# Kernel tuning notes

Measured on AMD Instinct MI355X. Metric: run time of the kernel, lower is better.

Reference implementation:

```python
import jax, jax.numpy as jnp
import numpy as np

EPS = 1e-8  # torch.nn.CosineSimilarity default eps
SCALE_WEIGHT = (1.0, 2.0, 3.0, 4.0)  # weight[idx] for 4 scales


def _nearest_labels(lab, H, W):
    # torch F.interpolate mode='nearest': src_idx = floor(dst_idx * in/out)
    H0, W0 = lab.shape[2], lab.shape[3]
    ri = (jnp.arange(H) * H0) // H
    ci = (jnp.arange(W) * W0) // W
    return lab[:, :, ri][:, :, :, ci]


def _scale_loss(pseudo_labels, feat, feat_old, num_class, num_old_class):
    B, C, H, W = feat.shape
    lab = _nearest_labels(pseudo_labels, H, W).reshape(-1)          # [B*H*W]
    f = jnp.transpose(feat, (0, 2, 3, 1)).reshape(-1, C)            # (b h w) c
    fo = jnp.transpose(feat_old, (0, 2, 3, 1)).reshape(-1, C)
    nf = jnp.maximum(jnp.sqrt(jnp.sum(f * f, axis=1)), EPS)
    nfo = jnp.maximum(jnp.sqrt(jnp.sum(fo * fo, axis=1)), EPS)
    sim = jnp.sum(f * fo, axis=1) / (nf * nfo)                      # per-pixel cosine
    # segment-reduce by class; label 255 (ignore) is out-of-range and dropped
    seg = jax.ops.segment_sum(sim, lab, num_segments=num_class)
    cnt = jax.ops.segment_sum(jnp.ones_like(sim), lab, num_segments=num_class)
    mean_sim = seg / jnp.maximum(cnt, 1.0)
    cls = jnp.arange(num_class)
    factor = jnp.where(cls == 0, num_old_class / num_class,
                       jnp.where(cls <= num_old_class, 1.0, 0.0))
    present = cnt > 0
    dis = 1.0 - mean_sim
    return jnp.sum(jnp.where(present, factor * dis, 0.0))


def setup_inputs() -> dict:
    key = jax.random.key(0)
    ks = jax.random.split(key, 9)
    B, C = 8, 256
    sizes = [(128, 128), (64, 64), (32, 32), (16, 16)]
    inp = {
        "pseudo_labels": jax.random.randint(ks[0], (B, 1, 512, 512), 0, 21, dtype=jnp.int64)
        if jax.config.jax_enable_x64 else
        jax.random.randint(ks[0], (B, 1, 512, 512), 0, 21).astype(jnp.int32),
    }
    for i, (h, w) in enumerate(sizes):
        inp[f"f{i}"] = jax.random.normal(ks[1 + i], (B, C, h, w), dtype=jnp.float32)
        inp[f"fo{i}"] = jax.random.normal(ks[5 + i], (B, C, h, w), dtype=jnp.float32)
    inp["num_class"] = 21
    inp["num_old_class"] = 15
    return inp


def reference(pseudo_labels, f0, f1, f2, f3, fo0, fo1, fo2, fo3, num_class, num_old_class):
    feats = (f0, f1, f2, f3)
    feats_old = (fo0, fo1, fo2, fo3)
    loss = jnp.float32(0.0)
    for idx in range(4):
        loss = loss + SCALE_WEIGHT[idx] * _scale_loss(
            pseudo_labels, feats[idx], feats_old[idx], num_class, num_old_class)
    return loss
```

## Files before the change

kernel.cpp:

```cpp
#include <hip/hip_runtime.h>
#include <math.h>


#define EPSV 1e-8f

__global__ __launch_bounds__(512)
void msrd_main(const float* __restrict__ f0, const float* __restrict__ fo0,
               const float* __restrict__ f1, const float* __restrict__ fo1,
               const float* __restrict__ f2, const float* __restrict__ fo2,
               const float* __restrict__ f3, const float* __restrict__ fo3,
               const int*   __restrict__ labels,
               const int*   __restrict__ p_nclass,
               float* __restrict__ ws)
{
    int bid = blockIdx.x;
    int scale, lb, logW, logHW, sshift;
    const float *f, *fo;
    if (bid < 1024)      { scale = 0; lb = bid;        f = f0; fo = fo0; logW = 7; logHW = 14; sshift = 2; }
    else if (bid < 1280) { scale = 1; lb = bid - 1024; f = f1; fo = fo1; logW = 6; logHW = 12; sshift = 3; }
    else if (bid < 1344) { scale = 2; lb = bid - 1280; f = f2; fo = fo2; logW = 5; logHW = 10; sshift = 4; }
    else                 { scale = 3; lb = bid - 1344; f = f3; fo = fo3; logW = 4; logHW = 8;  sshift = 5; }
    const int HW = 1 << logHW;
    const int W  = 1 << logW;

    const int tid  = threadIdx.x;
    const int wave = tid >> 6;
    const int lane = tid & 63;
    const int half = lane >> 5;
    const int gi   = lane & 31;

    const int g   = lb * 32 + gi;
    const int pix = g << 2;
    const int b   = pix >> logHW;
    const int rem = pix & (HW - 1);

    const int c0 = wave * 32 + half * 16;
    const float* __restrict__ fpb  = f  + (((size_t)(b * 256 + c0)) << logHW) + rem;
    const float* __restrict__ fopb = fo + (((size_t)(b * 256 + c0)) << logHW) + rem;

    float dx=0.f,dy=0.f,dz=0.f,dw=0.f;
    float ax=0.f,ay=0.f,az=0.f,aw=0.f;
    float bx=0.f,by=0.f,bz=0.f,bw=0.f;

    #pragma unroll
    for (int batch = 0; batch < 2; ++batch) {
        float4 X[8], Y[8];
        const size_t cb = (size_t)(batch * 8) << logHW;
        #pragma unroll
        for (int j = 0; j < 8; ++j)
            X[j] = *(const float4*)(fpb + cb + ((size_t)j << logHW));
        #pragma unroll
        for (int j = 0; j < 8; ++j)
            Y[j] = *(const float4*)(fopb + cb + ((size_t)j << logHW));
        #pragma unroll
        for (int j = 0; j < 8; ++j) {
            float4 x = X[j], y = Y[j];
            dx = fmaf(x.x, y.x, dx); dy = fmaf(x.y, y.y, dy);
            dz = fmaf(x.z, y.z, dz); dw = fmaf(x.w, y.w, dw);
            ax = fmaf(x.x, x.x, ax); ay = fmaf(x.y, x.y, ay);
            az = fmaf(x.z, x.z, az); aw = fmaf(x.w, x.w, aw);
            bx = fmaf(y.x, y.x, bx); by = fmaf(y.y, y.y, by);
            bz = fmaf(y.z, y.z, bz); bw = fmaf(y.w, y.w, bw);
        }
    }

    dx += __shfl_xor(dx, 32); dy += __shfl_xor(dy, 32);
    dz += __shfl_xor(dz, 32); dw += __shfl_xor(dw, 32);
    ax += __shfl_xor(ax, 32); ay += __shfl_xor(ay, 32);
    az += __shfl_xor(az, 32); aw += __shfl_xor(aw, 32);
    bx += __shfl_xor(bx, 32); by += __shfl_xor(by, 32);
    bz += __shfl_xor(bz, 32); bw += __shfl_xor(bw, 32);

    __shared__ float4 sD[8][32], sA[8][32], sB[8][32];
    __shared__ float bin_sim[32], bin_cnt[32];
    if (tid < 32) { bin_sim[tid] = 0.f; bin_cnt[tid] = 0.f; }
    if (half == 0) {
        sD[wave][gi] = make_float4(dx,dy,dz,dw);
        sA[wave][gi] = make_float4(ax,ay,az,aw);
        sB[wave][gi] = make_float4(bx,by,bz,bw);
    }
    __syncthreads();

    if (tid < 32) {
        float4 D = sD[0][gi], A = sA[0][gi], Bv = sB[0][gi];
        #pragma unroll
        for (int w = 1; w < 8; ++w) {
            float4 t;
            t = sD[w][gi]; D.x += t.x; D.y += t.y; D.z += t.z; D.w += t.w;
            t = sA[w][gi]; A.x += t.x; A.y += t.y; A.z += t.z; A.w += t.w;
            t = sB[w][gi]; Bv.x += t.x; Bv.y += t.y; Bv.z += t.z; Bv.w += t.w;
        }
        const int nclass  = *p_nclass;
        const int labbase = b << 18;
        float Dv[4] = {D.x, D.y, D.z, D.w};
        float Av[4] = {A.x, A.y, A.z, A.w};
        float Bw[4] = {Bv.x, Bv.y, Bv.z, Bv.w};
        #pragma unroll
        for (int j = 0; j < 4; ++j) {
            float na  = fmaxf(sqrtf(Av[j]), EPSV);
            float nb  = fmaxf(sqrtf(Bw[j]), EPSV);
            float sim = Dv[j] / (na * nb);
            int p    = rem + j;
            int h    = p >> logW;
            int col  = p & (W - 1);
            int lidx = labbase + ((h << sshift) << 9) + (col << sshift);
            int lab  = labels[lidx];
            if ((unsigned)lab < (unsigned)nclass) {
                atomicAdd(&bin_sim[lab], sim);
                atomicAdd(&bin_cnt[lab], 1.0f);
            }
        }
    }
    __syncthreads();

    if (tid < 32) {
        float s = bin_sim[tid], c = bin_cnt[tid];
        if (s != 0.f || c != 0.f) {
            atomicAdd(&ws[scale * 64 + tid],      s);
            atomicAdd(&ws[scale * 64 + 32 + tid], c);
        }
    }
}

__global__ void msrd_final(const float* __restrict__ ws,
                           const int* __restrict__ p_nclass,
                           const int* __restrict__ p_nold,
                           float* __restrict__ out)
{
    if (threadIdx.x == 0 && blockIdx.x == 0) {
        const int nc = *p_nclass;
        const int no = *p_nold;
        const float wgt[4] = {1.f, 2.f, 3.f, 4.f};
        float loss = 0.f;
        for (int s = 0; s < 4; ++s) {
            float sl = 0.f;
            for (int c = 0; c < nc && c < 32; ++c) {
                float seg = ws[s * 64 + c];
                float cnt = ws[s * 64 + 32 + c];
                if (cnt > 0.f) {
                    float factor = (c == 0) ? (float)no / (float)nc
                                            : (c <= no ? 1.f : 0.f);
                    sl += factor * (1.f - seg / fmaxf(cnt, 1.f));
                }
            }
            loss += wgt[s] * sl;
        }
        out[0] = loss;
    }
}

extern "C" void kernel_launch(void* const* d_in, const int* in_sizes, int n_in,
                              void* d_out, int out_size, void* d_ws, size_t ws_size,
                              hipStream_t stream) {
    const int*   labels = (const int*)  d_in[0];
    const float* f0  = (const float*)d_in[1];
    const float* fo0 = (const float*)d_in[2];
    const float* f1  = (const float*)d_in[3];
    const float* fo1 = (const float*)d_in[4];
    const float* f2  = (const float*)d_in[5];
    const float* fo2 = (const float*)d_in[6];
    const float* f3  = (const float*)d_in[7];
    const float* fo3 = (const float*)d_in[8];
    const int* p_nclass = (const int*)d_in[9];
    const int* p_nold   = (const int*)d_in[10];
    float* out = (float*)d_out;
    float* ws  = (float*)d_ws;

    hipMemsetAsync(ws, 0, 4 * 64 * sizeof(float), stream);
    msrd_main<<<dim3(1360), dim3(512), 0, stream>>>(f0, fo0, f1, fo1, f2, fo2, f3, fo3,
                                                    labels, p_nclass, ws);
    msrd_final<<<dim3(1), dim3(64), 0, stream>>>(ws, p_nclass, p_nold, out);
}
```

Baseline: 361.8 us.

## Halve block size, loop two channel passes per wave with smaller load batches

Each block now uses 256 threads, so every wave covers 32 channels in each of two passes instead of all channels being split across 8 waves. Loads are issued in groups of four float4 pairs with a scheduling barrier, and launch bounds request 6 waves per SIMD. The aim is lower register pressure and higher occupancy so that more memory requests are in flight. In exchange, each block has fewer loads outstanding at once and each thread carries more serial work.

```diff
diff --git a/kernel.cpp b/kernel.cpp
--- a/kernel.cpp
+++ b/kernel.cpp
@@ -4,7 +4,7 @@
 
 #define EPSV 1e-8f
 
-__global__ __launch_bounds__(512)
+__global__ __launch_bounds__(256, 6)
 void msrd_main(const float* __restrict__ f0, const float* __restrict__ fo0,
                const float* __restrict__ f1, const float* __restrict__ fo1,
                const float* __restrict__ f2, const float* __restrict__ fo2,
@@ -34,33 +34,55 @@
     const int b   = pix >> logHW;
     const int rem = pix & (HW - 1);
 
-    const int c0 = wave * 32 + half * 16;
-    const float* __restrict__ fpb  = f  + (((size_t)(b * 256 + c0)) << logHW) + rem;
-    const float* __restrict__ fopb = fo + (((size_t)(b * 256 + c0)) << logHW) + rem;
-
     float dx=0.f,dy=0.f,dz=0.f,dw=0.f;
     float ax=0.f,ay=0.f,az=0.f,aw=0.f;
     float bx=0.f,by=0.f,bz=0.f,bw=0.f;
 
     #pragma unroll
-    for (int batch = 0; batch < 2; ++batch) {
-        float4 X[8], Y[8];
-        const size_t cb = (size_t)(batch * 8) << logHW;
+    for (int pass = 0; pass < 2; ++pass) {
+        const int c0 = wave * 32 + half * 16 + pass * 128;
+        const float* __restrict__ fpb  = f  + (((size_t)(b * 256 + c0)) << logHW) + rem;
+        const float* __restrict__ fopb = fo + (((size_t)(b * 256 + c0)) << logHW) + rem;
         #pragma unroll
-        for (int j = 0; j < 8; ++j)
-            X[j] = *(const float4*)(fpb + cb + ((size_t)j << logHW));
-        #pragma unroll
-        for (int j = 0; j < 8; ++j)
-            Y[j] = *(const float4*)(fopb + cb + ((size_t)j << logHW));
-        #pragma unroll
-        for (int j = 0; j < 8; ++j) {
-            float4 x = X[j], y = Y[j];
-            dx = fmaf(x.x, y.x, dx); dy = fmaf(x.y, y.y, dy);
-            dz = fmaf(x.z, y.z, dz); dw = fmaf(x.w, y.w, dw);
-            ax = fmaf(x.x, x.x, ax); ay = fmaf(x.y, x.y, ay);
-            az = fmaf(x.z, x.z, az); aw = fmaf(x.w, x.w, aw);
-            bx = fmaf(y.x, y.x, bx); by = fmaf(y.y, y.y, by);
-            bz = fmaf(y.z, y.z, bz); bw = fmaf(y.w, y.w, bw);
+        for (int batch = 0; batch < 4; ++batch) {
+            const size_t cb = (size_t)(batch * 4) << logHW;
+            float4 X0, X1, X2, X3, Y0, Y1, Y2, Y3;
+            X0 = *(const float4*)(fpb  + cb);
+            X1 = *(const float4*)(fpb  + cb + ((size_t)1 << logHW));
+            X2 = *(const float4*)(fpb  + cb + ((size_t)2 << logHW));
+            X3 = *(const float4*)(fpb  + cb + ((size_t)3 << logHW));
+            Y0 = *(const float4*)(fopb + cb);
+            Y1 = *(const float4*)(fopb + cb + ((size_t)1 << logHW));
+            Y2 = *(const float4*)(fopb + cb + ((size_t)2 << logHW));
+            Y3 = *(const float4*)(fopb + cb + ((size_t)3 << logHW));
+            __builtin_amdgcn_sched_barrier(0);
+            dx = fmaf(X0.x, Y0.x, dx); dy = fmaf(X0.y, Y0.y, dy);
+            dz = fmaf(X0.z, Y0.z, dz); dw = fmaf(X0.w, Y0.w, dw);
+            ax = fmaf(X0.x, X0.x, ax); ay = fmaf(X0.y, X0.y, ay);
+            az = fmaf(X0.z, X0.z, az); aw = fmaf(X0.w, X0.w, aw);
+            bx = fmaf(Y0.x, Y0.x, bx); by = fmaf(Y0.y, Y0.y, by);
+            bz = fmaf(Y0.z, Y0.z, bz); bw = fmaf(Y0.w, Y0.w, bw);
+
+            dx = fmaf(X1.x, Y1.x, dx); dy = fmaf(X1.y, Y1.y, dy);
+            dz = fmaf(X1.z, Y1.z, dz); dw = fmaf(X1.w, Y1.w, dw);
+            ax = fmaf(X1.x, X1.x, ax); ay = fmaf(X1.y, X1.y, ay);
+            az = fmaf(X1.z, X1.z, az); aw = fmaf(X1.w, X1.w, aw);
+            bx = fmaf(Y1.x, Y1.x, bx); by = fmaf(Y1.y, Y1.y, by);
+            bz = fmaf(Y1.z, Y1.z, bz); bw = fmaf(Y1.w, Y1.w, bw);
+
+            dx = fmaf(X2.x, Y2.x, dx); dy = fmaf(X2.y, Y2.y, dy);
+            dz = fmaf(X2.z, Y2.z, dz); dw = fmaf(X2.w, Y2.w, dw);
+            ax = fmaf(X2.x, X2.x, ax); ay = fmaf(X2.y, X2.y, ay);
+            az = fmaf(X2.z, X2.z, az); aw = fmaf(X2.w, X2.w, aw);
+            bx = fmaf(Y2.x, Y2.x, bx); by = fmaf(Y2.y, Y2.y, by);
+            bz = fmaf(Y2.z, Y2.z, bz); bw = fmaf(Y2.w, Y2.w, bw);
+
+            dx = fmaf(X3.x, Y3.x, dx); dy = fmaf(X3.y, Y3.y, dy);
+            dz = fmaf(X3.z, Y3.z, dz); dw = fmaf(X3.w, Y3.w, dw);
+            ax = fmaf(X3.x, X3.x, ax); ay = fmaf(X3.y, X3.y, ay);
+            az = fmaf(X3.z, X3.z, az); aw = fmaf(X3.w, X3.w, aw);
+            bx = fmaf(Y3.x, Y3.x, bx); by = fmaf(Y3.y, Y3.y, by);
+            bz = fmaf(Y3.z, Y3.z, bz); bw = fmaf(Y3.w, Y3.w, bw);
         }
     }
 
@@ -71,7 +93,7 @@
     bx += __shfl_xor(bx, 32); by += __shfl_xor(by, 32);
     bz += __shfl_xor(bz, 32); bw += __shfl_xor(bw, 32);
 
-    __shared__ float4 sD[8][32], sA[8][32], sB[8][32];
+    __shared__ float4 sD[4][32], sA[4][32], sB[4][32];
     __shared__ float bin_sim[32], bin_cnt[32];
     if (tid < 32) { bin_sim[tid] = 0.f; bin_cnt[tid] = 0.f; }
     if (half == 0) {
@@ -84,7 +106,7 @@
     if (tid < 32) {
         float4 D = sD[0][gi], A = sA[0][gi], Bv = sB[0][gi];
         #pragma unroll
-        for (int w = 1; w < 8; ++w) {
+        for (int w = 1; w < 4; ++w) {
             float4 t;
             t = sD[w][gi]; D.x += t.x; D.y += t.y; D.z += t.z; D.w += t.w;
             t = sA[w][gi]; A.x += t.x; A.y += t.y; A.z += t.z; A.w += t.w;
@@ -167,7 +189,7 @@
     float* ws  = (float*)d_ws;
 
     hipMemsetAsync(ws, 0, 4 * 64 * sizeof(float), stream);
-    msrd_main<<<dim3(1360), dim3(512), 0, stream>>>(f0, fo0, f1, fo1, f2, fo2, f3, fo3,
+    msrd_main<<<dim3(1360), dim3(256), 0, stream>>>(f0, fo0, f1, fo1, f2, fo2, f3, fo3,
                                                     labels, p_nclass, ws);
     msrd_final<<<dim3(1), dim3(64), 0, stream>>>(ws, p_nclass, p_nold, out);
 }
```

Measured after the change: 387.1 us. +7.0%, slower.

## Assign one pixel per thread with full channel loop, drop cross-wave reduction

Applied to the files above, without the earlier changes.

Each block of 128 threads now handles 128 pixels, with every thread looping over all 256 channels using scalar coalesced loads. The old scheme split 16 channels per half-wave with float4 loads and combined partials through a shuffle and a shared-memory reduction. That reduction, its shared arrays and the serial 32-thread epilogue are removed, and every thread computes its cosine and does the label atomic itself. In exchange each thread runs a long dependent loop with less memory-level parallelism per block and uses narrower scalar loads. It also makes many more shared-memory atomics per block, which can contend because there are only 21 classes.

```diff
diff --git a/kernel.cpp b/kernel.cpp
--- a/kernel.cpp
+++ b/kernel.cpp
@@ -4,7 +4,7 @@
 
 #define EPSV 1e-8f
 
-__global__ __launch_bounds__(512)
+__global__ __launch_bounds__(128)
 void msrd_main(const float* __restrict__ f0, const float* __restrict__ fo0,
                const float* __restrict__ f1, const float* __restrict__ fo1,
                const float* __restrict__ f2, const float* __restrict__ fo2,
@@ -13,102 +13,59 @@
                const int*   __restrict__ p_nclass,
                float* __restrict__ ws)
 {
-    int bid = blockIdx.x;
+    const int bid = blockIdx.x;
     int scale, lb, logW, logHW, sshift;
     const float *f, *fo;
     if (bid < 1024)      { scale = 0; lb = bid;        f = f0; fo = fo0; logW = 7; logHW = 14; sshift = 2; }
     else if (bid < 1280) { scale = 1; lb = bid - 1024; f = f1; fo = fo1; logW = 6; logHW = 12; sshift = 3; }
     else if (bid < 1344) { scale = 2; lb = bid - 1280; f = f2; fo = fo2; logW = 5; logHW = 10; sshift = 4; }
     else                 { scale = 3; lb = bid - 1344; f = f3; fo = fo3; logW = 4; logHW = 8;  sshift = 5; }
-    const int HW = 1 << logHW;
-    const int W  = 1 << logW;
+    const int W   = 1 << logW;
+    const int HW  = 1 << logHW;
+    const int tid = threadIdx.x;
 
-    const int tid  = threadIdx.x;
-    const int wave = tid >> 6;
-    const int lane = tid & 63;
-    const int half = lane >> 5;
-    const int gi   = lane & 31;
-
-    const int g   = lb * 32 + gi;
-    const int pix = g << 2;
+    const int pix = lb * 128 + tid;
     const int b   = pix >> logHW;
     const int rem = pix & (HW - 1);
 
-    const int c0 = wave * 32 + half * 16;
-    const float* __restrict__ fpb  = f  + (((size_t)(b * 256 + c0)) << logHW) + rem;
-    const float* __restrict__ fopb = fo + (((size_t)(b * 256 + c0)) << logHW) + rem;
+    const float* __restrict__ fp  = f  + (((size_t)(b * 256)) << logHW) + rem;
+    const float* __restrict__ fop = fo + (((size_t)(b * 256)) << logHW) + rem;
+    const size_t cs = (size_t)HW;
 
-    float dx=0.f,dy=0.f,dz=0.f,dw=0.f;
-    float ax=0.f,ay=0.f,az=0.f,aw=0.f;
-    float bx=0.f,by=0.f,bz=0.f,bw=0.f;
+    float d = 0.f, a = 0.f, bn = 0.f;
 
-    #pragma unroll
-    for (int batch = 0; batch < 2; ++batch) {
-        float4 X[8], Y[8];
-        const size_t cb = (size_t)(batch * 8) << logHW;
+    for (int it = 0; it < 32; ++it) {
+        float X[8], Y[8];
         #pragma unroll
-        for (int j = 0; j < 8; ++j)
-            X[j] = *(const float4*)(fpb + cb + ((size_t)j << logHW));
+        for (int j = 0; j < 8; ++j) X[j] = fp[(size_t)j * cs];
         #pragma unroll
-        for (int j = 0; j < 8; ++j)
-            Y[j] = *(const float4*)(fopb + cb + ((size_t)j << logHW));
+        for (int j = 0; j < 8; ++j) Y[j] = fop[(size_t)j * cs];
         #pragma unroll
         for (int j = 0; j < 8; ++j) {
-            float4 x = X[j], y = Y[j];
-            dx = fmaf(x.x, y.x, dx); dy = fmaf(x.y, y.y, dy);
-            dz = fmaf(x.z, y.z, dz); dw = fmaf(x.w, y.w, dw);
-            ax = fmaf(x.x, x.x, ax); ay = fmaf(x.y, x.y, ay);
-            az = fmaf(x.z, x.z, az); aw = fmaf(x.w, x.w, aw);
-            bx = fmaf(y.x, y.x, bx); by = fmaf(y.y, y.y, by);
-            bz = fmaf(y.z, y.z, bz); bw = fmaf(y.w, y.w, bw);
+            d  = fmaf(X[j], Y[j], d);
+            a  = fmaf(X[j], X[j], a);
+            bn = fmaf(Y[j], Y[j], bn);
         }
+        fp  += cs * 8;
+        fop += cs * 8;
     }
 
-    dx += __shfl_xor(dx, 32); dy += __shfl_xor(dy, 32);
-    dz += __shfl_xor(dz, 32); dw += __shfl_xor(dw, 32);
-    ax += __shfl_xor(ax, 32); ay += __shfl_xor(ay, 32);
-    az += __shfl_xor(az, 32); aw += __shfl_xor(aw, 32);
-    bx += __shfl_xor(bx, 32); by += __shfl_xor(by, 32);
-    bz += __shfl_xor(bz, 32); bw += __shfl_xor(bw, 32);
-
-    __shared__ float4 sD[8][32], sA[8][32], sB[8][32];
     __shared__ float bin_sim[32], bin_cnt[32];
     if (tid < 32) { bin_sim[tid] = 0.f; bin_cnt[tid] = 0.f; }
-    if (half == 0) {
-        sD[wave][gi] = make_float4(dx,dy,dz,dw);
-        sA[wave][gi] = make_float4(ax,ay,az,aw);
-        sB[wave][gi] = make_float4(bx,by,bz,bw);
-    }
     __syncthreads();
 
-    if (tid < 32) {
-        float4 D = sD[0][gi], A = sA[0][gi], Bv = sB[0][gi];
-        #pragma unroll
-        for (int w = 1; w < 8; ++w) {
-            float4 t;
-            t = sD[w][gi]; D.x += t.x; D.y += t.y; D.z += t.z; D.w += t.w;
-            t = sA[w][gi]; A.x += t.x; A.y += t.y; A.z += t.z; A.w += t.w;
-            t = sB[w][gi]; Bv.x += t.x; Bv.y += t.y; Bv.z += t.z; Bv.w += t.w;
-        }
-        const int nclass  = *p_nclass;
-        const int labbase = b << 18;
-        float Dv[4] = {D.x, D.y, D.z, D.w};
-        float Av[4] = {A.x, A.y, A.z, A.w};
-        float Bw[4] = {Bv.x, Bv.y, Bv.z, Bv.w};
-        #pragma unroll
-        for (int j = 0; j < 4; ++j) {
-            float na  = fmaxf(sqrtf(Av[j]), EPSV);
-            float nb  = fmaxf(sqrtf(Bw[j]), EPSV);
-            float sim = Dv[j] / (na * nb);
-            int p    = rem + j;
-            int h    = p >> logW;
-            int col  = p & (W - 1);
-            int lidx = labbase + ((h << sshift) << 9) + (col << sshift);
-            int lab  = labels[lidx];
-            if ((unsigned)lab < (unsigned)nclass) {
-                atomicAdd(&bin_sim[lab], sim);
-                atomicAdd(&bin_cnt[lab], 1.0f);
-            }
+    {
+        float na  = fmaxf(sqrtf(a),  EPSV);
+        float nb  = fmaxf(sqrtf(bn), EPSV);
+        float sim = d / (na * nb);
+        const int h   = rem >> logW;
+        const int col = rem & (W - 1);
+        const int lidx = (b << 18) + ((h << sshift) << 9) + (col << sshift);
+        const int lab  = labels[lidx];
+        const int nclass = *p_nclass;
+        if ((unsigned)lab < (unsigned)(nclass < 32 ? nclass : 32)) {
+            atomicAdd(&bin_sim[lab], sim);
+            atomicAdd(&bin_cnt[lab], 1.0f);
         }
     }
     __syncthreads();
@@ -167,7 +124,7 @@
     float* ws  = (float*)d_ws;
 
     hipMemsetAsync(ws, 0, 4 * 64 * sizeof(float), stream);
-    msrd_main<<<dim3(1360), dim3(512), 0, stream>>>(f0, fo0, f1, fo1, f2, fo2, f3, fo3,
+    msrd_main<<<dim3(1360), dim3(128), 0, stream>>>(f0, fo0, f1, fo1, f2, fo2, f3, fo3,
                                                     labels, p_nclass, ws);
     msrd_final<<<dim3(1), dim3(64), 0, stream>>>(ws, p_nclass, p_nold, out);
 }
```

Result: slower. 436.2 us (+20.6%).

## Halve block size and software-pipeline channel loads with double-buffered registers

Applied to the files above, without the earlier changes.

Each block now uses 256 threads instead of 512, and every thread covers 32 channels in two 16-channel halves instead of 16 channels. The load loop becomes a double-buffered register pipeline: the next batch of float4 loads is issued before the current batch is consumed, with sched_barriers keeping that order. The cross-wave reduction in shared memory shrinks from 8 to 4 slots. The aim is to keep more memory requests in flight per wave and to halve the cross-wave reduction work. In exchange, total threads in flight drop and per-thread register pressure rises, which may reduce the ability to hide latency.

```diff
diff --git a/kernel.cpp b/kernel.cpp
--- a/kernel.cpp
+++ b/kernel.cpp
@@ -3,8 +3,31 @@
 
 
 #define EPSV 1e-8f
+#define SBAR() __builtin_amdgcn_sched_barrier(0)
 
-__global__ __launch_bounds__(512)
+#define LOAD_BATCH(X0_,X1_,X2_,X3_,Y0_,Y1_,Y2_,Y3_, koff)                    \
+  { const float* _pf = fpb + (koff); const float* _pq = fopb + (koff);       \
+    X0_ = *(const float4*)(_pf);                                             \
+    X1_ = *(const float4*)(_pf + cs);                                        \
+    X2_ = *(const float4*)(_pf + 2*cs);                                      \
+    X3_ = *(const float4*)(_pf + 3*cs);                                      \
+    Y0_ = *(const float4*)(_pq);                                             \
+    Y1_ = *(const float4*)(_pq + cs);                                        \
+    Y2_ = *(const float4*)(_pq + 2*cs);                                      \
+    Y3_ = *(const float4*)(_pq + 3*cs); }
+
+#define FMA1(Xv,Yv)                                                          \
+    dx = fmaf(Xv.x, Yv.x, dx); dy = fmaf(Xv.y, Yv.y, dy);                    \
+    dz = fmaf(Xv.z, Yv.z, dz); dw = fmaf(Xv.w, Yv.w, dw);                    \
+    ax = fmaf(Xv.x, Xv.x, ax); ay = fmaf(Xv.y, Xv.y, ay);                    \
+    az = fmaf(Xv.z, Xv.z, az); aw = fmaf(Xv.w, Xv.w, aw);                    \
+    bx = fmaf(Yv.x, Yv.x, bx); by = fmaf(Yv.y, Yv.y, by);                    \
+    bz = fmaf(Yv.z, Yv.z, bz); bw = fmaf(Yv.w, Yv.w, bw);
+
+#define CONSUME(X0_,X1_,X2_,X3_,Y0_,Y1_,Y2_,Y3_)                             \
+    FMA1(X0_, Y0_) FMA1(X1_, Y1_) FMA1(X2_, Y2_) FMA1(X3_, Y3_)
+
+__global__ __launch_bounds__(256, 2)
 void msrd_main(const float* __restrict__ f0, const float* __restrict__ fo0,
                const float* __restrict__ f1, const float* __restrict__ fo1,
                const float* __restrict__ f2, const float* __restrict__ fo2,
@@ -37,32 +60,31 @@
     const int c0 = wave * 32 + half * 16;
     const float* __restrict__ fpb  = f  + (((size_t)(b * 256 + c0)) << logHW) + rem;
     const float* __restrict__ fopb = fo + (((size_t)(b * 256 + c0)) << logHW) + rem;
+    const size_t cs = (size_t)HW;
 
     float dx=0.f,dy=0.f,dz=0.f,dw=0.f;
     float ax=0.f,ay=0.f,az=0.f,aw=0.f;
     float bx=0.f,by=0.f,bz=0.f,bw=0.f;
 
-    #pragma unroll
-    for (int batch = 0; batch < 2; ++batch) {
-        float4 X[8], Y[8];
-        const size_t cb = (size_t)(batch * 8) << logHW;
-        #pragma unroll
-        for (int j = 0; j < 8; ++j)
-            X[j] = *(const float4*)(fpb + cb + ((size_t)j << logHW));
-        #pragma unroll
-        for (int j = 0; j < 8; ++j)
-            Y[j] = *(const float4*)(fopb + cb + ((size_t)j << logHW));
-        #pragma unroll
-        for (int j = 0; j < 8; ++j) {
-            float4 x = X[j], y = Y[j];
-            dx = fmaf(x.x, y.x, dx); dy = fmaf(x.y, y.y, dy);
-            dz = fmaf(x.z, y.z, dz); dw = fmaf(x.w, y.w, dw);
-            ax = fmaf(x.x, x.x, ax); ay = fmaf(x.y, x.y, ay);
-            az = fmaf(x.z, x.z, az); aw = fmaf(x.w, x.w, aw);
-            bx = fmaf(y.x, y.x, bx); by = fmaf(y.y, y.y, by);
-            bz = fmaf(y.z, y.z, bz); bw = fmaf(y.w, y.w, bw);
-        }
-    }
+    float4 AX0,AX1,AX2,AX3, AY0,AY1,AY2,AY3;
+    float4 BX0,BX1,BX2,BX3, BY0,BY1,BY2,BY3;
+
+    LOAD_BATCH(AX0,AX1,AX2,AX3, AY0,AY1,AY2,AY3, (size_t)0);        SBAR();
+    LOAD_BATCH(BX0,BX1,BX2,BX3, BY0,BY1,BY2,BY3, (size_t)4*cs);     SBAR();
+    CONSUME(AX0,AX1,AX2,AX3, AY0,AY1,AY2,AY3);                      SBAR();
+    LOAD_BATCH(AX0,AX1,AX2,AX3, AY0,AY1,AY2,AY3, (size_t)8*cs);     SBAR();
+    CONSUME(BX0,BX1,BX2,BX3, BY0,BY1,BY2,BY3);                      SBAR();
+    LOAD_BATCH(BX0,BX1,BX2,BX3, BY0,BY1,BY2,BY3, (size_t)12*cs);    SBAR();
+    CONSUME(AX0,AX1,AX2,AX3, AY0,AY1,AY2,AY3);                      SBAR();
+    LOAD_BATCH(AX0,AX1,AX2,AX3, AY0,AY1,AY2,AY3, (size_t)128*cs);   SBAR();
+    CONSUME(BX0,BX1,BX2,BX3, BY0,BY1,BY2,BY3);                      SBAR();
+    LOAD_BATCH(BX0,BX1,BX2,BX3, BY0,BY1,BY2,BY3, (size_t)132*cs);   SBAR();
+    CONSUME(AX0,AX1,AX2,AX3, AY0,AY1,AY2,AY3);                      SBAR();
+    LOAD_BATCH(AX0,AX1,AX2,AX3, AY0,AY1,AY2,AY3, (size_t)136*cs);   SBAR();
+    CONSUME(BX0,BX1,BX2,BX3, BY0,BY1,BY2,BY3);                      SBAR();
+    LOAD_BATCH(BX0,BX1,BX2,BX3, BY0,BY1,BY2,BY3, (size_t)140*cs);   SBAR();
+    CONSUME(AX0,AX1,AX2,AX3, AY0,AY1,AY2,AY3);                      SBAR();
+    CONSUME(BX0,BX1,BX2,BX3, BY0,BY1,BY2,BY3);
 
     dx += __shfl_xor(dx, 32); dy += __shfl_xor(dy, 32);
     dz += __shfl_xor(dz, 32); dw += __shfl_xor(dw, 32);
@@ -71,7 +93,7 @@
     bx += __shfl_xor(bx, 32); by += __shfl_xor(by, 32);
     bz += __shfl_xor(bz, 32); bw += __shfl_xor(bw, 32);
 
-    __shared__ float4 sD[8][32], sA[8][32], sB[8][32];
+    __shared__ float4 sD[4][32], sA[4][32], sB[4][32];
     __shared__ float bin_sim[32], bin_cnt[32];
     if (tid < 32) { bin_sim[tid] = 0.f; bin_cnt[tid] = 0.f; }
     if (half == 0) {
@@ -84,7 +106,7 @@
     if (tid < 32) {
         float4 D = sD[0][gi], A = sA[0][gi], Bv = sB[0][gi];
         #pragma unroll
-        for (int w = 1; w < 8; ++w) {
+        for (int w = 1; w < 4; ++w) {
             float4 t;
             t = sD[w][gi]; D.x += t.x; D.y += t.y; D.z += t.z; D.w += t.w;
             t = sA[w][gi]; A.x += t.x; A.y += t.y; A.z += t.z; A.w += t.w;
@@ -167,7 +189,7 @@
     float* ws  = (float*)d_ws;
 
     hipMemsetAsync(ws, 0, 4 * 64 * sizeof(float), stream);
-    msrd_main<<<dim3(1360), dim3(512), 0, stream>>>(f0, fo0, f1, fo1, f2, fo2, f3, fo3,
+    msrd_main<<<dim3(1360), dim3(256), 0, stream>>>(f0, fo0, f1, fo1, f2, fo2, f3, fo3,
                                                     labels, p_nclass, ws);
     msrd_final<<<dim3(1), dim3(64), 0, stream>>>(ws, p_nclass, p_nold, out);
 }
```

Measured after the change: 360.9 us. No clear change (-0.2%).
